# Optimization experiments

Hardware: AMD Instinct MI355X
Metric: run time of the kernel (lower is better)

Reference implementation:

```python
import jax, jax.numpy as jnp
import numpy as np

IN_FEATURES = 1024
NUM_EXPERTS = 64
TOP_K = 2


def setup_inputs() -> dict:
    key = jax.random.key(0)
    kx, kw, kb = jax.random.split(key, 3)
    x = jax.random.normal(kx, (8, 4096, IN_FEATURES), dtype=jnp.float32)
    # nn.Linear init scale ~ 1/sqrt(in_features)
    bound = 1.0 / np.sqrt(IN_FEATURES)
    W = jax.random.uniform(kw, (NUM_EXPERTS, IN_FEATURES), dtype=jnp.float32, minval=-bound, maxval=bound)
    b = jax.random.uniform(kb, (NUM_EXPERTS,), dtype=jnp.float32, minval=-bound, maxval=bound)
    return {"x": x, "W": W, "b": b}


def reference(x, W, b):
    # logits: [B, S, E]
    logits = jnp.einsum("bsd,ed->bse", x, W) + b
    gates = jax.nn.softmax(logits, axis=-1)
    top_k_gates, top_k_indices = jax.lax.top_k(gates, TOP_K)
    return top_k_gates, top_k_indices
```

## Files before the change

kernel.cpp:

```cpp
#include <hip/hip_runtime.h>

#define D 1024
#define E 64
#define TPB 256
#define TOKS 64
#define KSTEPS 32

typedef __attribute__((ext_vector_type(8))) short bf16x8;
typedef __attribute__((ext_vector_type(8))) unsigned short u16x8;
typedef __attribute__((ext_vector_type(4))) float f32x4;
typedef __attribute__((ext_vector_type(4))) unsigned int u32x4;

__device__ __forceinline__ unsigned short bf16_rne(float f) {
    unsigned u = __builtin_bit_cast(unsigned, f);
    u += 0x7fffu + ((u >> 16) & 1u);
    return (unsigned short)(u >> 16);
}
__device__ __forceinline__ float bf16_to_f(unsigned short h) {
    unsigned u = ((unsigned)h) << 16;
    return __builtin_bit_cast(float, u);
}
__device__ __forceinline__ unsigned cvt_pk_bf16(float a, float b) {
    unsigned r;
    asm("v_cvt_pk_bf16_f32 %0, %1, %2" : "=v"(r) : "v"(a), "v"(b));
    return r;
}
__device__ __forceinline__ float lo_val(unsigned p) {
    return __builtin_bit_cast(float, p << 16);
}
__device__ __forceinline__ float hi_val(unsigned p) {
    return __builtin_bit_cast(float, p & 0xffff0000u);
}

struct Afrag { f32x4 u, v; };
struct Bfrag { bf16x8 f0, f1, f2, f3, f4, f5, f6, f7; };

__device__ __forceinline__ void split8_rne(f32x4 a, f32x4 b, bf16x8& hv, bf16x8& lv) {
    unsigned h0 = cvt_pk_bf16(a[0], a[1]);
    unsigned h1 = cvt_pk_bf16(a[2], a[3]);
    unsigned h2 = cvt_pk_bf16(b[0], b[1]);
    unsigned h3 = cvt_pk_bf16(b[2], b[3]);
    unsigned l0 = cvt_pk_bf16(a[0] - lo_val(h0), a[1] - hi_val(h0));
    unsigned l1 = cvt_pk_bf16(a[2] - lo_val(h1), a[3] - hi_val(h1));
    unsigned l2 = cvt_pk_bf16(b[0] - lo_val(h2), b[1] - hi_val(h2));
    unsigned l3 = cvt_pk_bf16(b[2] - lo_val(h3), b[3] - hi_val(h3));
    hv = __builtin_bit_cast(bf16x8, (u32x4){h0, h1, h2, h3});
    lv = __builtin_bit_cast(bf16x8, (u32x4){l0, l1, l2, l3});
}

__global__ __launch_bounds__(TPB) void router_prep(
        const float* __restrict__ W, unsigned short* __restrict__ Ws) {
    int t = blockIdx.x * TPB + threadIdx.x;
    int lane = t & 63;
    int nt = (t >> 6) & 3;
    int ks = t >> 8;
    int n = lane & 15, q = lane >> 4;
    const float* src = W + (size_t)(nt * 16 + n) * D + ks * 32 + q * 8;
    u16x8 hv, lv;
#pragma unroll
    for (int j = 0; j < 8; ++j) {
        float v = src[j];
        unsigned short h = bf16_rne(v);
        hv[j] = h;
        lv[j] = bf16_rne(v - bf16_to_f(h));
    }
    size_t base = ((size_t)(ks * 8 + nt * 2) * 64 + lane) * 8;
    *(u16x8*)(Ws + base)          = hv;
    *(u16x8*)(Ws + base + 64 * 8) = lv;
}

__global__ __launch_bounds__(TPB, 2) void router_main(
        const float* __restrict__ x, const unsigned short* __restrict__ Ws,
        const float* __restrict__ bias, float* __restrict__ out, int T) {
    __shared__ __align__(16) float ls[TOKS][E + 1];

    const int tid  = threadIdx.x;
    const int lane = tid & 63;
    const int wid  = tid >> 6;
    const int n    = lane & 15;
    const int q    = lane >> 4;
    const int t0   = blockIdx.x * TOKS;

    const float* arow = x + (size_t)(t0 + wid * 16 + n) * D + q * 8;
    const bf16x8* bptr = (const bf16x8*)Ws + lane;

    f32x4 c0 = {0.f, 0.f, 0.f, 0.f}, c1 = c0, c2 = c0, c3 = c0;
    bf16x8 ah, al;

#define LOADA(A_, ks_) do {                                   \
        A_.u = *(const f32x4*)(arow + (ks_) * 32);            \
        A_.v = *(const f32x4*)(arow + (ks_) * 32 + 4);        \
    } while (0)

#define LOADB(B_, ks_) do {                                   \
        const bf16x8* _p = bptr + (size_t)(ks_) * 512;        \
        B_.f0 = _p[0];   B_.f1 = _p[64];  B_.f2 = _p[128];    \
        B_.f3 = _p[192]; B_.f4 = _p[256]; B_.f5 = _p[320];    \
        B_.f6 = _p[384]; B_.f7 = _p[448];                     \
    } while (0)

#define MFMA __builtin_amdgcn_mfma_f32_16x16x32_bf16
#define COMP(B_) do {                                                       \
        c0 = MFMA(ah, B_.f0, c0, 0, 0, 0);                                  \
        c0 = MFMA(al, B_.f0, c0, 0, 0, 0);                                  \
        c0 = MFMA(ah, B_.f1, c0, 0, 0, 0);                                  \
        c1 = MFMA(ah, B_.f2, c1, 0, 0, 0);                                  \
        c1 = MFMA(al, B_.f2, c1, 0, 0, 0);                                  \
        c1 = MFMA(ah, B_.f3, c1, 0, 0, 0);                                  \
        c2 = MFMA(ah, B_.f4, c2, 0, 0, 0);                                  \
        c2 = MFMA(al, B_.f4, c2, 0, 0, 0);                                  \
        c2 = MFMA(ah, B_.f5, c2, 0, 0, 0);                                  \
        c3 = MFMA(ah, B_.f6, c3, 0, 0, 0);                                  \
        c3 = MFMA(al, B_.f6, c3, 0, 0, 0);                                  \
        c3 = MFMA(ah, B_.f7, c3, 0, 0, 0);                                  \
    } while (0)

#define STEP(ks_, Ause_, Afill_, Buse_, Bfill_) do {          \
        LOADB(Bfill_, (ks_) + 2);                             \
        LOADA(Afill_, (ks_) + 3);                             \
        split8_rne(Ause_.u, Ause_.v, ah, al);                 \
        COMP(Buse_);                                          \
    } while (0)

    Afrag A0, A1, A2, A3;
    Bfrag B0, B1, B2, B3;

    LOADA(A0, 0); LOADA(A1, 1); LOADA(A2, 2);
    LOADB(B0, 0); LOADB(B1, 1);

    for (int kb = 0; kb < KSTEPS - 4; kb += 4) {
        STEP(kb + 0, A0, A3, B0, B2);
        STEP(kb + 1, A1, A0, B1, B3);
        STEP(kb + 2, A2, A1, B2, B0);
        STEP(kb + 3, A3, A2, B3, B1);
    }

    LOADB(B2, 30); LOADA(A3, 31);
    split8_rne(A0.u, A0.v, ah, al); COMP(B0);
    LOADB(B3, 31);
    split8_rne(A1.u, A1.v, ah, al); COMP(B1);
    split8_rne(A2.u, A2.v, ah, al); COMP(B2);
    split8_rne(A3.u, A3.v, ah, al); COMP(B3);

    {
        const int row = wid * 16 + q * 4;
#define STORE_C(c_, nt_) do {                                 \
            int col = (nt_) * 16 + n;                         \
            float bv = bias[col];                             \
            ls[row + 0][col] = c_[0] + bv;                    \
            ls[row + 1][col] = c_[1] + bv;                    \
            ls[row + 2][col] = c_[2] + bv;                    \
            ls[row + 3][col] = c_[3] + bv;                    \
        } while (0)
        STORE_C(c0, 0); STORE_C(c1, 1); STORE_C(c2, 2); STORE_C(c3, 3);
#undef STORE_C
    }
    __syncthreads();

    if (tid < TOKS) {
        float m1 = -3.4e38f, m2 = -3.4e38f;
        int i1 = 0, i2 = 0;
        for (int e = 0; e < E; ++e) {
            float v = ls[tid][e];
            if (v > m1) { m2 = m1; i2 = i1; m1 = v; i1 = e; }
            else if (v > m2) { m2 = v; i2 = e; }
        }
        float Z = 0.f;
        for (int e = 0; e < E; ++e) Z += __expf(ls[tid][e] - m1);
        float inv = 1.f / Z;
        int gt = t0 + tid;
        out[(size_t)gt * 2]     = inv;
        out[(size_t)gt * 2 + 1] = __expf(m2 - m1) * inv;
        float* oi = out + (size_t)T * 2;
        oi[(size_t)gt * 2]     = (float)i1;
        oi[(size_t)gt * 2 + 1] = (float)i2;
    }
}

extern "C" void kernel_launch(void* const* d_in, const int* in_sizes, int n_in,
                              void* d_out, int out_size, void* d_ws, size_t ws_size,
                              hipStream_t stream) {
    const float* x = (const float*)d_in[0];
    const float* W = (const float*)d_in[1];
    const float* b = (const float*)d_in[2];
    float* out = (float*)d_out;
    unsigned short* Ws = (unsigned short*)d_ws;
    int T = in_sizes[0] / D;
    hipLaunchKernelGGL(router_prep, dim3(32), dim3(TPB), 0, stream, W, Ws);
    hipLaunchKernelGGL(router_main, dim3(T / TOKS), dim3(TPB), 0, stream,
                       x, Ws, b, out, T);
}
```

Measured before the change: 218.0 us.

## Stage split W fragments through LDS in phases instead of per-wave global loads

Each block now cooperatively copies an eight-kstep slab of the pre-split bf16 W into shared memory per phase, and the four waves read their B fragments from LDS. Before, every wave loaded the same B fragments from global/L2 on its own. The change cuts redundant global traffic for W by four within a block. In exchange it adds two barriers per phase, uses more LDS (64KB union), drops the deep register prefetch of B, and lets the A-prefetch depth shrink to two steps, which may expose load latency and limit occupancy.

After: 212.7 us. -2.4%, faster.

```diff
diff --git a/kernel.cpp b/kernel.cpp
--- a/kernel.cpp
+++ b/kernel.cpp
@@ -5,6 +5,8 @@
 #define TPB 256
 #define TOKS 64
 #define KSTEPS 32
+#define PH_KS 8
+#define PHASES 4
 
 typedef __attribute__((ext_vector_type(8))) short bf16x8;
 typedef __attribute__((ext_vector_type(8))) unsigned short u16x8;
@@ -72,7 +74,10 @@
 __global__ __launch_bounds__(TPB, 2) void router_main(
         const float* __restrict__ x, const unsigned short* __restrict__ Ws,
         const float* __restrict__ bias, float* __restrict__ out, int T) {
-    __shared__ __align__(16) float ls[TOKS][E + 1];
+    __shared__ __align__(16) union SM {
+        unsigned short w[PH_KS * 8 * 64 * 8];
+        float ls[TOKS][E + 1];
+    } sm;
 
     const int tid  = threadIdx.x;
     const int lane = tid & 63;
@@ -82,75 +87,90 @@
     const int t0   = blockIdx.x * TOKS;
 
     const float* arow = x + (size_t)(t0 + wid * 16 + n) * D + q * 8;
-    const bf16x8* bptr = (const bf16x8*)Ws + lane;
 
     f32x4 c0 = {0.f, 0.f, 0.f, 0.f}, c1 = c0, c2 = c0, c3 = c0;
     bf16x8 ah, al;
+    Afrag A0, A1;
+    Bfrag Bt;
 
 #define LOADA(A_, ks_) do {                                   \
         A_.u = *(const f32x4*)(arow + (ks_) * 32);            \
         A_.v = *(const f32x4*)(arow + (ks_) * 32 + 4);        \
     } while (0)
 
-#define LOADB(B_, ks_) do {                                   \
-        const bf16x8* _p = bptr + (size_t)(ks_) * 512;        \
-        B_.f0 = _p[0];   B_.f1 = _p[64];  B_.f2 = _p[128];    \
-        B_.f3 = _p[192]; B_.f4 = _p[256]; B_.f5 = _p[320];    \
-        B_.f6 = _p[384]; B_.f7 = _p[448];                     \
+#define LDSB(kk_) do {                                                      \
+        const bf16x8* _qq = (const bf16x8*)sm.w + (kk_) * 512 + lane;       \
+        Bt.f0 = _qq[0];   Bt.f1 = _qq[64];  Bt.f2 = _qq[128];               \
+        Bt.f3 = _qq[192]; Bt.f4 = _qq[256]; Bt.f5 = _qq[320];               \
+        Bt.f6 = _qq[384]; Bt.f7 = _qq[448];                                 \
     } while (0)
 
 #define MFMA __builtin_amdgcn_mfma_f32_16x16x32_bf16
-#define COMP(B_) do {                                                       \
-        c0 = MFMA(ah, B_.f0, c0, 0, 0, 0);                                  \
-        c0 = MFMA(al, B_.f0, c0, 0, 0, 0);                                  \
-        c0 = MFMA(ah, B_.f1, c0, 0, 0, 0);                                  \
-        c1 = MFMA(ah, B_.f2, c1, 0, 0, 0);                                  \
-        c1 = MFMA(al, B_.f2, c1, 0, 0, 0);                                  \
-        c1 = MFMA(ah, B_.f3, c1, 0, 0, 0);                                  \
-        c2 = MFMA(ah, B_.f4, c2, 0, 0, 0);                                  \
-        c2 = MFMA(al, B_.f4, c2, 0, 0, 0);                                  \
-        c2 = MFMA(ah, B_.f5, c2, 0, 0, 0);                                  \
-        c3 = MFMA(ah, B_.f6, c3, 0, 0, 0);                                  \
-        c3 = MFMA(al, B_.f6, c3, 0, 0, 0);                                  \
-        c3 = MFMA(ah, B_.f7, c3, 0, 0, 0);                                  \
+#define COMP() do {                                                         \
+        c0 = MFMA(ah, Bt.f0, c0, 0, 0, 0);                                  \
+        c0 = MFMA(al, Bt.f0, c0, 0, 0, 0);                                  \
+        c0 = MFMA(ah, Bt.f1, c0, 0, 0, 0);                                  \
+        c1 = MFMA(ah, Bt.f2, c1, 0, 0, 0);                                  \
+        c1 = MFMA(al, Bt.f2, c1, 0, 0, 0);                                  \
+        c1 = MFMA(ah, Bt.f3, c1, 0, 0, 0);                                  \
+        c2 = MFMA(ah, Bt.f4, c2, 0, 0, 0);                                  \
+        c2 = MFMA(al, Bt.f4, c2, 0, 0, 0);                                  \
+        c2 = MFMA(ah, Bt.f5, c2, 0, 0, 0);                                  \
+        c3 = MFMA(ah, Bt.f6, c3, 0, 0, 0);                                  \
+        c3 = MFMA(al, Bt.f6, c3, 0, 0, 0);                                  \
+        c3 = MFMA(ah, Bt.f7, c3, 0, 0, 0);                                  \
     } while (0)
 
-#define STEP(ks_, Ause_, Afill_, Buse_, Bfill_) do {          \
-        LOADB(Bfill_, (ks_) + 2);                             \
-        LOADA(Afill_, (ks_) + 3);                             \
-        split8_rne(Ause_.u, Ause_.v, ah, al);                 \
-        COMP(Buse_);                                          \
-    } while (0)
-
-    Afrag A0, A1, A2, A3;
-    Bfrag B0, B1, B2, B3;
-
-    LOADA(A0, 0); LOADA(A1, 1); LOADA(A2, 2);
-    LOADB(B0, 0); LOADB(B1, 1);
-
-    for (int kb = 0; kb < KSTEPS - 4; kb += 4) {
-        STEP(kb + 0, A0, A3, B0, B2);
-        STEP(kb + 1, A1, A0, B1, B3);
-        STEP(kb + 2, A2, A1, B2, B0);
-        STEP(kb + 3, A3, A2, B3, B1);
-    }
-
-    LOADB(B2, 30); LOADA(A3, 31);
-    split8_rne(A0.u, A0.v, ah, al); COMP(B0);
-    LOADB(B3, 31);
-    split8_rne(A1.u, A1.v, ah, al); COMP(B1);
-    split8_rne(A2.u, A2.v, ah, al); COMP(B2);
-    split8_rne(A3.u, A3.v, ah, al); COMP(B3);
+    LOADA(A0, 0);
+    LOADA(A1, 1);
+
+    const u32x4* gws = (const u32x4*)Ws + tid;
+    u32x4* lws = (u32x4*)sm.w + tid;
+
+    for (int p = 0; p < PHASES; ++p) {
+        const int ksb = p * PH_KS;
+        {
+            const u32x4* g = gws + p * 4096;
+            u32x4 s0 = g[0],    s1 = g[256],  s2 = g[512],  s3 = g[768];
+            u32x4 s4 = g[1024], s5 = g[1280], s6 = g[1536], s7 = g[1792];
+            lws[0]    = s0; lws[256]  = s1; lws[512]  = s2; lws[768]  = s3;
+            lws[1024] = s4; lws[1280] = s5; lws[1536] = s6; lws[1792] = s7;
+            u32x4 s8  = g[2048], s9  = g[2304], s10 = g[2560], s11 = g[2816];
+            u32x4 s12 = g[3072], s13 = g[3328], s14 = g[3584], s15 = g[3840];
+            lws[2048] = s8;  lws[2304] = s9;  lws[2560] = s10; lws[2816] = s11;
+            lws[3072] = s12; lws[3328] = s13; lws[3584] = s14; lws[3840] = s15;
+        }
+        __syncthreads();
+
+#pragma unroll
+        for (int kk = 0; kk < PH_KS; kk += 2) {
+            {
+                split8_rne(A0.u, A0.v, ah, al);
+                int kpre = ksb + kk + 2; if (kpre > KSTEPS - 1) kpre = KSTEPS - 1;
+                LOADA(A0, kpre);
+                LDSB(kk);
+                COMP();
+            }
+            {
+                split8_rne(A1.u, A1.v, ah, al);
+                int kpre = ksb + kk + 3; if (kpre > KSTEPS - 1) kpre = KSTEPS - 1;
+                LOADA(A1, kpre);
+                LDSB(kk + 1);
+                COMP();
+            }
+        }
+        __syncthreads();
+    }
 
     {
         const int row = wid * 16 + q * 4;
 #define STORE_C(c_, nt_) do {                                 \
             int col = (nt_) * 16 + n;                         \
             float bv = bias[col];                             \
-            ls[row + 0][col] = c_[0] + bv;                    \
-            ls[row + 1][col] = c_[1] + bv;                    \
-            ls[row + 2][col] = c_[2] + bv;                    \
-            ls[row + 3][col] = c_[3] + bv;                    \
+            sm.ls[row + 0][col] = c_[0] + bv;                 \
+            sm.ls[row + 1][col] = c_[1] + bv;                 \
+            sm.ls[row + 2][col] = c_[2] + bv;                 \
+            sm.ls[row + 3][col] = c_[3] + bv;                 \
         } while (0)
         STORE_C(c0, 0); STORE_C(c1, 1); STORE_C(c2, 2); STORE_C(c3, 3);
 #undef STORE_C
@@ -161,12 +181,12 @@
         float m1 = -3.4e38f, m2 = -3.4e38f;
         int i1 = 0, i2 = 0;
         for (int e = 0; e < E; ++e) {
-            float v = ls[tid][e];
+            float v = sm.ls[tid][e];
             if (v > m1) { m2 = m1; i2 = i1; m1 = v; i1 = e; }
             else if (v > m2) { m2 = v; i2 = e; }
         }
         float Z = 0.f;
-        for (int e = 0; e < E; ++e) Z += __expf(ls[tid][e] - m1);
+        for (int e = 0; e < E; ++e) Z += __expf(sm.ls[tid][e] - m1);
         float inv = 1.f / Z;
         int gt = t0 + tid;
         out[(size_t)gt * 2]     = inv;
```

## Split K across waves with fewer tokens per block and LDS reduction

Applied to the files above, without the earlier changes.

Each block now handles 16 tokens instead of 64. Its four waves each cover one quarter of the K dimension and reduce their partial logits in shared memory before the softmax/top-2 stage. This quadruples the block count and raises the occupancy hint, so there is more parallelism to hide memory latency. In exchange each block re-reads the whole split weight tensor for only 16 tokens, adds an LDS reduction pass and an extra barrier, shortens the software pipeline, and leaves only 16 of 256 threads active in the top-k tail.

Measured after the change: 227.6 us. 4.4% more time.

```diff
diff --git a/kernel.cpp b/kernel.cpp
--- a/kernel.cpp
+++ b/kernel.cpp
@@ -3,8 +3,8 @@
 #define D 1024
 #define E 64
 #define TPB 256
-#define TOKS 64
-#define KSTEPS 32
+#define TOKS 16
+#define KSW 8
 
 typedef __attribute__((ext_vector_type(8))) short bf16x8;
 typedef __attribute__((ext_vector_type(8))) unsigned short u16x8;
@@ -69,10 +69,12 @@
     *(u16x8*)(Ws + base + 64 * 8) = lv;
 }
 
-__global__ __launch_bounds__(TPB, 2) void router_main(
+__global__ __launch_bounds__(TPB, 4) void router_main(
         const float* __restrict__ x, const unsigned short* __restrict__ Ws,
         const float* __restrict__ bias, float* __restrict__ out, int T) {
-    __shared__ __align__(16) float ls[TOKS][E + 1];
+    __shared__ __align__(16) float part[4][TOKS][E];
+    __shared__ float ls[TOKS][E + 1];
+    __shared__ float sbias[E];
 
     const int tid  = threadIdx.x;
     const int lane = tid & 63;
@@ -80,80 +82,88 @@
     const int n    = lane & 15;
     const int q    = lane >> 4;
     const int t0   = blockIdx.x * TOKS;
-
-    const float* arow = x + (size_t)(t0 + wid * 16 + n) * D + q * 8;
+    const int kb   = wid * KSW;
+
+    if (tid < E) sbias[tid] = bias[tid];
+
+    const float* arow = x + (size_t)(t0 + n) * D + q * 8;
     const bf16x8* bptr = (const bf16x8*)Ws + lane;
 
     f32x4 c0 = {0.f, 0.f, 0.f, 0.f}, c1 = c0, c2 = c0, c3 = c0;
     bf16x8 ah, al;
+    Afrag A0, A1;
+    Bfrag Bt;
 
 #define LOADA(A_, ks_) do {                                   \
         A_.u = *(const f32x4*)(arow + (ks_) * 32);            \
         A_.v = *(const f32x4*)(arow + (ks_) * 32 + 4);        \
     } while (0)
 
-#define LOADB(B_, ks_) do {                                   \
+#define LOADB(ks_) do {                                       \
         const bf16x8* _p = bptr + (size_t)(ks_) * 512;        \
-        B_.f0 = _p[0];   B_.f1 = _p[64];  B_.f2 = _p[128];    \
-        B_.f3 = _p[192]; B_.f4 = _p[256]; B_.f5 = _p[320];    \
-        B_.f6 = _p[384]; B_.f7 = _p[448];                     \
+        Bt.f0 = _p[0];   Bt.f1 = _p[64];  Bt.f2 = _p[128];    \
+        Bt.f3 = _p[192]; Bt.f4 = _p[256]; Bt.f5 = _p[320];    \
+        Bt.f6 = _p[384]; Bt.f7 = _p[448];                     \
     } while (0)
 
 #define MFMA __builtin_amdgcn_mfma_f32_16x16x32_bf16
-#define COMP(B_) do {                                                       \
-        c0 = MFMA(ah, B_.f0, c0, 0, 0, 0);                                  \
-        c0 = MFMA(al, B_.f0, c0, 0, 0, 0);                                  \
-        c0 = MFMA(ah, B_.f1, c0, 0, 0, 0);                                  \
-        c1 = MFMA(ah, B_.f2, c1, 0, 0, 0);                                  \
-        c1 = MFMA(al, B_.f2, c1, 0, 0, 0);                                  \
-        c1 = MFMA(ah, B_.f3, c1, 0, 0, 0);                                  \
-        c2 = MFMA(ah, B_.f4, c2, 0, 0, 0);                                  \
-        c2 = MFMA(al, B_.f4, c2, 0, 0, 0);                                  \
-        c2 = MFMA(ah, B_.f5, c2, 0, 0, 0);                                  \
-        c3 = MFMA(ah, B_.f6, c3, 0, 0, 0);                                  \
-        c3 = MFMA(al, B_.f6, c3, 0, 0, 0);                                  \
-        c3 = MFMA(ah, B_.f7, c3, 0, 0, 0);                                  \
+#define COMP() do {                                           \
+        c0 = MFMA(ah, Bt.f0, c0, 0, 0, 0);                    \
+        c0 = MFMA(al, Bt.f0, c0, 0, 0, 0);                    \
+        c0 = MFMA(ah, Bt.f1, c0, 0, 0, 0);                    \
+        c1 = MFMA(ah, Bt.f2, c1, 0, 0, 0);                    \
+        c1 = MFMA(al, Bt.f2, c1, 0, 0, 0);                    \
+        c1 = MFMA(ah, Bt.f3, c1, 0, 0, 0);                    \
+        c2 = MFMA(ah, Bt.f4, c2, 0, 0, 0);                    \
+        c2 = MFMA(al, Bt.f4, c2, 0, 0, 0);                    \
+        c2 = MFMA(ah, Bt.f5, c2, 0, 0, 0);                    \
+        c3 = MFMA(ah, Bt.f6, c3, 0, 0, 0);                    \
+        c3 = MFMA(al, Bt.f6, c3, 0, 0, 0);                    \
+        c3 = MFMA(ah, Bt.f7, c3, 0, 0, 0);                    \
     } while (0)
 
-#define STEP(ks_, Ause_, Afill_, Buse_, Bfill_) do {          \
-        LOADB(Bfill_, (ks_) + 2);                             \
-        LOADA(Afill_, (ks_) + 3);                             \
-        split8_rne(Ause_.u, Ause_.v, ah, al);                 \
-        COMP(Buse_);                                          \
-    } while (0)
-
-    Afrag A0, A1, A2, A3;
-    Bfrag B0, B1, B2, B3;
-
-    LOADA(A0, 0); LOADA(A1, 1); LOADA(A2, 2);
-    LOADB(B0, 0); LOADB(B1, 1);
-
-    for (int kb = 0; kb < KSTEPS - 4; kb += 4) {
-        STEP(kb + 0, A0, A3, B0, B2);
-        STEP(kb + 1, A1, A0, B1, B3);
-        STEP(kb + 2, A2, A1, B2, B0);
-        STEP(kb + 3, A3, A2, B3, B1);
-    }
-
-    LOADB(B2, 30); LOADA(A3, 31);
-    split8_rne(A0.u, A0.v, ah, al); COMP(B0);
-    LOADB(B3, 31);
-    split8_rne(A1.u, A1.v, ah, al); COMP(B1);
-    split8_rne(A2.u, A2.v, ah, al); COMP(B2);
-    split8_rne(A3.u, A3.v, ah, al); COMP(B3);
+    LOADA(A0, kb + 0);
+    LOADA(A1, kb + 1);
+
+#pragma unroll
+    for (int kk = 0; kk < KSW; kk += 2) {
+        {
+            LOADB(kb + kk);
+            split8_rne(A0.u, A0.v, ah, al);
+            const int kr = (kk + 2 < KSW) ? kk + 2 : KSW - 1;
+            LOADA(A0, kb + kr);
+            COMP();
+        }
+        {
+            LOADB(kb + kk + 1);
+            split8_rne(A1.u, A1.v, ah, al);
+            const int kr = (kk + 3 < KSW) ? kk + 3 : KSW - 1;
+            LOADA(A1, kb + kr);
+            COMP();
+        }
+    }
 
     {
-        const int row = wid * 16 + q * 4;
-#define STORE_C(c_, nt_) do {                                 \
+        const int row = q * 4;
+#define STORE_P(c_, nt_) do {                                 \
             int col = (nt_) * 16 + n;                         \
-            float bv = bias[col];                             \
-            ls[row + 0][col] = c_[0] + bv;                    \
-            ls[row + 1][col] = c_[1] + bv;                    \
-            ls[row + 2][col] = c_[2] + bv;                    \
-            ls[row + 3][col] = c_[3] + bv;                    \
+            part[wid][row + 0][col] = c_[0];                  \
+            part[wid][row + 1][col] = c_[1];                  \
+            part[wid][row + 2][col] = c_[2];                  \
+            part[wid][row + 3][col] = c_[3];                  \
         } while (0)
-        STORE_C(c0, 0); STORE_C(c1, 1); STORE_C(c2, 2); STORE_C(c3, 3);
-#undef STORE_C
+        STORE_P(c0, 0); STORE_P(c1, 1); STORE_P(c2, 2); STORE_P(c3, 3);
+#undef STORE_P
+    }
+    __syncthreads();
+
+#pragma unroll
+    for (int j = 0; j < 4; ++j) {
+        int idx = tid + j * TPB;
+        int tok = idx >> 6, e = idx & 63;
+        float s = ((part[0][tok][e] + part[1][tok][e]) + part[2][tok][e])
+                  + part[3][tok][e];
+        ls[tok][e] = s + sbias[e];
     }
     __syncthreads();
 
```

## Stage split-bf16 weight chunks through double-buffered LDS instead of per-wave global loads

Applied to the files above, without the earlier changes.

Before, each of the four waves loaded all weight fragments from global memory (L2) itself. Now the block loads the preprocessed W in 32KB chunks cooperatively into a double-buffered LDS region, with register prefetch of the next chunk and a barrier per chunk. The x loads are grouped by chunk, and the bias is cached in LDS. This cuts redundant global weight traffic per block, at the cost of 64KB LDS (lower occupancy, launch bound of 2 dropped) and barriers in the main loop.

Measured after the change: 204.0 us. 1.07x faster.

```diff
diff --git a/kernel.cpp b/kernel.cpp
--- a/kernel.cpp
+++ b/kernel.cpp
@@ -4,7 +4,8 @@
 #define E 64
 #define TPB 256
 #define TOKS 64
-#define KSTEPS 32
+#define NCH 8
+#define CHB 32768
 
 typedef __attribute__((ext_vector_type(8))) short bf16x8;
 typedef __attribute__((ext_vector_type(8))) unsigned short u16x8;
@@ -31,9 +32,6 @@
 __device__ __forceinline__ float hi_val(unsigned p) {
     return __builtin_bit_cast(float, p & 0xffff0000u);
 }
-
-struct Afrag { f32x4 u, v; };
-struct Bfrag { bf16x8 f0, f1, f2, f3, f4, f5, f6, f7; };
 
 __device__ __forceinline__ void split8_rne(f32x4 a, f32x4 b, bf16x8& hv, bf16x8& lv) {
     unsigned h0 = cvt_pk_bf16(a[0], a[1]);
@@ -48,9 +46,9 @@
     lv = __builtin_bit_cast(bf16x8, (u32x4){l0, l1, l2, l3});
 }
 
-__global__ __launch_bounds__(TPB) void router_prep(
+__global__ __launch_bounds__(256) void router_prep(
         const float* __restrict__ W, unsigned short* __restrict__ Ws) {
-    int t = blockIdx.x * TPB + threadIdx.x;
+    int t = blockIdx.x * 256 + threadIdx.x;
     int lane = t & 63;
     int nt = (t >> 6) & 3;
     int ks = t >> 8;
@@ -69,10 +67,14 @@
     *(u16x8*)(Ws + base + 64 * 8) = lv;
 }
 
-__global__ __launch_bounds__(TPB, 2) void router_main(
+__global__ __launch_bounds__(TPB) void router_main(
         const float* __restrict__ x, const unsigned short* __restrict__ Ws,
         const float* __restrict__ bias, float* __restrict__ out, int T) {
-    __shared__ __align__(16) float ls[TOKS][E + 1];
+    __shared__ __align__(16) union SM {
+        unsigned char buf[2][CHB];
+        float ls[TOKS][E + 1];
+    } sm;
+    __shared__ float sbias[E];
 
     const int tid  = threadIdx.x;
     const int lane = tid & 63;
@@ -81,76 +83,106 @@
     const int q    = lane >> 4;
     const int t0   = blockIdx.x * TOKS;
 
+    if (tid < E) sbias[tid] = bias[tid];
+
     const float* arow = x + (size_t)(t0 + wid * 16 + n) * D + q * 8;
-    const bf16x8* bptr = (const bf16x8*)Ws + lane;
+    const u32x4* gws  = (const u32x4*)Ws;
 
     f32x4 c0 = {0.f, 0.f, 0.f, 0.f}, c1 = c0, c2 = c0, c3 = c0;
-    bf16x8 ah, al;
-
-#define LOADA(A_, ks_) do {                                   \
-        A_.u = *(const f32x4*)(arow + (ks_) * 32);            \
-        A_.v = *(const f32x4*)(arow + (ks_) * 32 + 4);        \
-    } while (0)
-
-#define LOADB(B_, ks_) do {                                   \
-        const bf16x8* _p = bptr + (size_t)(ks_) * 512;        \
-        B_.f0 = _p[0];   B_.f1 = _p[64];  B_.f2 = _p[128];    \
-        B_.f3 = _p[192]; B_.f4 = _p[256]; B_.f5 = _p[320];    \
-        B_.f6 = _p[384]; B_.f7 = _p[448];                     \
+
+    u32x4 W0, W1, W2, W3, W4, W5, W6, W7;
+    f32x4 A0u, A0v, A1u, A1v, A2u, A2v, A3u, A3v;
+    f32x4 N0u, N0v, N1u, N1v, N2u, N2v, N3u, N3v;
+
+#define ISSUEW(c_) do {                                               \
+        const u32x4* _g = gws + (size_t)(c_) * 2048 + tid;            \
+        W0 = _g[0];    W1 = _g[256];  W2 = _g[512];  W3 = _g[768];    \
+        W4 = _g[1024]; W5 = _g[1280]; W6 = _g[1536]; W7 = _g[1792];   \
+    } while (0)
+
+#define WRITEW(bi_) do {                                              \
+        u32x4* _l = (u32x4*)sm.buf[bi_] + tid;                        \
+        _l[0]    = W0; _l[256]  = W1; _l[512]  = W2; _l[768]  = W3;   \
+        _l[1024] = W4; _l[1280] = W5; _l[1536] = W6; _l[1792] = W7;   \
+    } while (0)
+
+#define ISSUEA(p0u,p0v,p1u,p1v,p2u,p2v,p3u,p3v, c_) do {              \
+        const float* _b = arow + (size_t)(c_) * 128;                  \
+        p0u = *(const f32x4*)(_b);       p0v = *(const f32x4*)(_b + 4);   \
+        p1u = *(const f32x4*)(_b + 32);  p1v = *(const f32x4*)(_b + 36);  \
+        p2u = *(const f32x4*)(_b + 64);  p2v = *(const f32x4*)(_b + 68);  \
+        p3u = *(const f32x4*)(_b + 96);  p3v = *(const f32x4*)(_b + 100); \
     } while (0)
 
 #define MFMA __builtin_amdgcn_mfma_f32_16x16x32_bf16
-#define COMP(B_) do {                                                       \
-        c0 = MFMA(ah, B_.f0, c0, 0, 0, 0);                                  \
-        c0 = MFMA(al, B_.f0, c0, 0, 0, 0);                                  \
-        c0 = MFMA(ah, B_.f1, c0, 0, 0, 0);                                  \
-        c1 = MFMA(ah, B_.f2, c1, 0, 0, 0);                                  \
-        c1 = MFMA(al, B_.f2, c1, 0, 0, 0);                                  \
-        c1 = MFMA(ah, B_.f3, c1, 0, 0, 0);                                  \
-        c2 = MFMA(ah, B_.f4, c2, 0, 0, 0);                                  \
-        c2 = MFMA(al, B_.f4, c2, 0, 0, 0);                                  \
-        c2 = MFMA(ah, B_.f5, c2, 0, 0, 0);                                  \
-        c3 = MFMA(ah, B_.f6, c3, 0, 0, 0);                                  \
-        c3 = MFMA(al, B_.f6, c3, 0, 0, 0);                                  \
-        c3 = MFMA(ah, B_.f7, c3, 0, 0, 0);                                  \
-    } while (0)
-
-#define STEP(ks_, Ause_, Afill_, Buse_, Bfill_) do {          \
-        LOADB(Bfill_, (ks_) + 2);                             \
-        LOADA(Afill_, (ks_) + 3);                             \
-        split8_rne(Ause_.u, Ause_.v, ah, al);                 \
-        COMP(Buse_);                                          \
-    } while (0)
-
-    Afrag A0, A1, A2, A3;
-    Bfrag B0, B1, B2, B3;
-
-    LOADA(A0, 0); LOADA(A1, 1); LOADA(A2, 2);
-    LOADB(B0, 0); LOADB(B1, 1);
-
-    for (int kb = 0; kb < KSTEPS - 4; kb += 4) {
-        STEP(kb + 0, A0, A3, B0, B2);
-        STEP(kb + 1, A1, A0, B1, B3);
-        STEP(kb + 2, A2, A1, B2, B0);
-        STEP(kb + 3, A3, A2, B3, B1);
-    }
-
-    LOADB(B2, 30); LOADA(A3, 31);
-    split8_rne(A0.u, A0.v, ah, al); COMP(B0);
-    LOADB(B3, 31);
-    split8_rne(A1.u, A1.v, ah, al); COMP(B1);
-    split8_rne(A2.u, A2.v, ah, al); COMP(B2);
-    split8_rne(A3.u, A3.v, ah, al); COMP(B3);
+#define COMPSTEP(bi_, ksl_, au_, av_) do {                            \
+        bf16x8 ah, al;                                                \
+        split8_rne(au_, av_, ah, al);                                 \
+        const char* _p = (const char*)sm.buf[bi_] + (ksl_) * 8192 + lane * 16; \
+        {                                                             \
+            bf16x8 bh = *(const bf16x8*)(_p);                         \
+            bf16x8 bl = *(const bf16x8*)(_p + 1024);                  \
+            c0 = MFMA(ah, bh, c0, 0, 0, 0);                           \
+            c0 = MFMA(al, bh, c0, 0, 0, 0);                           \
+            c0 = MFMA(ah, bl, c0, 0, 0, 0);                           \
+        }                                                             \
+        {                                                             \
+            bf16x8 bh = *(const bf16x8*)(_p + 2048);                  \
+            bf16x8 bl = *(const bf16x8*)(_p + 3072);                  \
+            c1 = MFMA(ah, bh, c1, 0, 0, 0);                           \
+            c1 = MFMA(al, bh, c1, 0, 0, 0);                           \
+            c1 = MFMA(ah, bl, c1, 0, 0, 0);                           \
+        }                                                             \
+        {                                                             \
+            bf16x8 bh = *(const bf16x8*)(_p + 4096);                  \
+            bf16x8 bl = *(const bf16x8*)(_p + 5120);                  \
+            c2 = MFMA(ah, bh, c2, 0, 0, 0);                           \
+            c2 = MFMA(al, bh, c2, 0, 0, 0);                           \
+            c2 = MFMA(ah, bl, c2, 0, 0, 0);                           \
+        }                                                             \
+        {                                                             \
+            bf16x8 bh = *(const bf16x8*)(_p + 6144);                  \
+            bf16x8 bl = *(const bf16x8*)(_p + 7168);                  \
+            c3 = MFMA(ah, bh, c3, 0, 0, 0);                           \
+            c3 = MFMA(al, bh, c3, 0, 0, 0);                           \
+            c3 = MFMA(ah, bl, c3, 0, 0, 0);                           \
+        }                                                             \
+    } while (0)
+
+#define COMPCHUNK(bi_, p0u,p0v,p1u,p1v,p2u,p2v,p3u,p3v) do {          \
+        COMPSTEP(bi_, 0, p0u, p0v);                                   \
+        COMPSTEP(bi_, 1, p1u, p1v);                                   \
+        COMPSTEP(bi_, 2, p2u, p2v);                                   \
+        COMPSTEP(bi_, 3, p3u, p3v);                                   \
+    } while (0)
+
+    ISSUEW(0);
+    ISSUEA(A0u,A0v,A1u,A1v,A2u,A2v,A3u,A3v, 0);
+    WRITEW(0);
+    __syncthreads();
+
+    for (int c = 0; c < NCH; c += 2) {
+        ISSUEW(c + 1);
+        ISSUEA(N0u,N0v,N1u,N1v,N2u,N2v,N3u,N3v, c + 1);
+        COMPCHUNK(0, A0u,A0v,A1u,A1v,A2u,A2v,A3u,A3v);
+        WRITEW(1);
+        __syncthreads();
+        ISSUEW((c + 2) & (NCH - 1));
+        ISSUEA(A0u,A0v,A1u,A1v,A2u,A2v,A3u,A3v, (c + 2) & (NCH - 1));
+        COMPCHUNK(1, N0u,N0v,N1u,N1v,N2u,N2v,N3u,N3v);
+        WRITEW(0);
+        __syncthreads();
+    }
 
     {
         const int row = wid * 16 + q * 4;
-#define STORE_C(c_, nt_) do {                                 \
-            int col = (nt_) * 16 + n;                         \
-            float bv = bias[col];                             \
-            ls[row + 0][col] = c_[0] + bv;                    \
-            ls[row + 1][col] = c_[1] + bv;                    \
-            ls[row + 2][col] = c_[2] + bv;                    \
-            ls[row + 3][col] = c_[3] + bv;                    \
+#define STORE_C(c_, nt_) do {                                         \
+            int col = (nt_) * 16 + n;                                 \
+            float bv = sbias[col];                                    \
+            sm.ls[row + 0][col] = c_[0] + bv;                         \
+            sm.ls[row + 1][col] = c_[1] + bv;                         \
+            sm.ls[row + 2][col] = c_[2] + bv;                         \
+            sm.ls[row + 3][col] = c_[3] + bv;                         \
         } while (0)
         STORE_C(c0, 0); STORE_C(c1, 1); STORE_C(c2, 2); STORE_C(c3, 3);
 #undef STORE_C
@@ -161,12 +193,12 @@
         float m1 = -3.4e38f, m2 = -3.4e38f;
         int i1 = 0, i2 = 0;
         for (int e = 0; e < E; ++e) {
-            float v = ls[tid][e];
+            float v = sm.ls[tid][e];
             if (v > m1) { m2 = m1; i2 = i1; m1 = v; i1 = e; }
             else if (v > m2) { m2 = v; i2 = e; }
         }
         float Z = 0.f;
-        for (int e = 0; e < E; ++e) Z += __expf(ls[tid][e] - m1);
+        for (int e = 0; e < E; ++e) Z += __expf(sm.ls[tid][e] - m1);
         float inv = 1.f / Z;
         int gt = t0 + tid;
         out[(size_t)gt * 2]     = inv;
@@ -186,7 +218,7 @@
     float* out = (float*)d_out;
     unsigned short* Ws = (unsigned short*)d_ws;
     int T = in_sizes[0] / D;
-    hipLaunchKernelGGL(router_prep, dim3(32), dim3(TPB), 0, stream, W, Ws);
+    hipLaunchKernelGGL(router_prep, dim3(32), dim3(256), 0, stream, W, Ws);
     hipLaunchKernelGGL(router_main, dim3(T / TOKS), dim3(TPB), 0, stream,
                        x, Ws, b, out, T);
 }
```
